# Kernel optimization log

Measured on AMD Instinct MI355X. Metric: run time of the kernel, lower is better.

Reference implementation:

```python
import jax, jax.numpy as jnp
import numpy as np

DIM = 1280
N_HEADS = 10
HEAD_DIM = 128
BASE = 10000.0
BATCH = 2
SEQ = 2048


def _rope(x):
    # x: [b, h, s, d]; matches source: split even/odd channels, rotate, concat halves
    b, h, s, d = x.shape
    theta = 1.0 / (BASE ** (jnp.arange(0, d, 2, dtype=jnp.float32) / d))  # [d/2]
    ang = jnp.arange(s, dtype=jnp.float32)[:, None] * theta               # [s, d/2]
    cos = jnp.cos(ang)
    sin = jnp.sin(ang)
    x1 = x[..., 0::2]
    x2 = x[..., 1::2]
    return jnp.concatenate([x1 * cos - x2 * sin, x1 * sin + x2 * cos], axis=-1)


def setup_inputs() -> dict:
    key = jax.random.key(0)
    ks = jax.random.split(key, 6)
    w_std = 0.02
    x = jax.random.normal(ks[0], (BATCH, SEQ, DIM), dtype=jnp.float32)
    positions = jnp.arange(SEQ, dtype=jnp.int64 if jax.config.jax_enable_x64 else jnp.int32)
    Wq = jax.random.normal(ks[1], (DIM, DIM), dtype=jnp.float32) * w_std
    Wk = jax.random.normal(ks[2], (DIM, DIM), dtype=jnp.float32) * w_std
    Wv = jax.random.normal(ks[3], (DIM, DIM), dtype=jnp.float32) * w_std
    Wo = jax.random.normal(ks[4], (DIM, DIM), dtype=jnp.float32) * w_std
    bq = jnp.zeros((DIM,), jnp.float32)
    bk = jnp.zeros((DIM,), jnp.float32)
    bv = jnp.zeros((DIM,), jnp.float32)
    bo = jnp.zeros((DIM,), jnp.float32)
    return {"x": x, "positions": positions, "Wq": Wq, "bq": bq, "Wk": Wk,
            "bk": bk, "Wv": Wv, "bv": bv, "Wo": Wo, "bo": bo}


def reference(x, positions, Wq, bq, Wk, bk, Wv, bv, Wo, bo):
    b, s, _ = x.shape
    scale = 1.0 / np.sqrt(HEAD_DIM)

    def proj(W, bias):
        y = jnp.einsum('bsd,ed->bse', x, W) + bias  # Linear: x @ W^T + b
        return y.reshape(b, s, N_HEADS, HEAD_DIM).transpose(0, 2, 1, 3)

    q = _rope(proj(Wq, bq))  # [b, h, s, hd]
    k = _rope(proj(Wk, bk))
    v = proj(Wv, bv)

    scores = jnp.einsum('bhqd,bhkd->bhqk', q, k) * scale
    causal = jnp.tril(jnp.ones((s, s), dtype=bool))
    scores = jnp.where(causal, scores, jnp.float32(-jnp.inf))
    attn = jax.nn.softmax(scores, axis=-1)
    out = jnp.einsum('bhqk,bhkd->bhqd', attn, v)
    out = out.transpose(0, 2, 1, 3).reshape(b, s, N_HEADS * HEAD_DIM)
    return jnp.einsum('bse,de->bsd', out, Wo) + bo
```

## Files before the change

### kernel.cpp

```cpp
#include <hip/hip_runtime.h>
#include <cmath>

typedef unsigned short u16;
typedef __attribute__((ext_vector_type(8))) short bf16x8;
typedef __attribute__((ext_vector_type(4))) float f32x4;

#define B_    2
#define SEQ_  2048
#define NH_   10
#define HD_   128
#define DIM_  1280

__device__ __forceinline__ u16 f2bf(float f) {
    union { float f; unsigned u; } v; v.f = f;
    unsigned r = (v.u + 0x7fffu + ((v.u >> 16) & 1u)) >> 16;
    return (u16)r;
}
__device__ __forceinline__ float bf2f(u16 h) {
    union { unsigned u; float f; } v; v.u = ((unsigned)h) << 16;
    return v.f;
}
__device__ __forceinline__ f32x4 mfma16(bf16x8 a, bf16x8 b, f32x4 c) {
    return __builtin_amdgcn_mfma_f32_16x16x32_bf16(a, b, c, 0, 0, 0);
}
__device__ __forceinline__ void g2l16(const void* g, void* l) {
    __builtin_amdgcn_global_load_lds(
        (const __attribute__((address_space(1))) unsigned*)g,
        (__attribute__((address_space(3))) unsigned*)l, 16, 0, 0);
}
__device__ __forceinline__ ushort4 pack4(float a, float b, float c, float d) {
    ushort4 w; w.x = f2bf(a); w.y = f2bf(b); w.z = f2bf(c); w.w = f2bf(d);
    return w;
}

__global__ __launch_bounds__(256) void cvt_k(const float* __restrict__ x,
                                             const float* __restrict__ w0,
                                             const float* __restrict__ w1,
                                             const float* __restrict__ w2,
                                             const float* __restrict__ w3,
                                             u16* __restrict__ xb,
                                             u16* __restrict__ d0,
                                             u16* __restrict__ d1,
                                             u16* __restrict__ d2,
                                             u16* __restrict__ d3,
                                             float* __restrict__ ct,
                                             float* __restrict__ st) {
    const int NX = B_ * SEQ_ * DIM_;
    const int WN = DIM_ * DIM_;
    const int NCV = (NX + 4 * WN) / 8 / 256;
    int bid = blockIdx.x;
    if (bid >= NCV) {
        int idx = (bid - NCV) * 256 + threadIdx.x;
        int s = idx >> 6, j = idx & 63;
        float e = (float)j * (1.0f / 64.0f);
        float theta = 1.0f / powf(10000.0f, e);
        float ang = (float)s * theta;
        ct[idx] = cosf(ang);
        st[idx] = sinf(ang);
        return;
    }
    int i = (bid * 256 + threadIdx.x) * 8;
    const float* src; u16* dst; int off;
    if (i < NX) { src = x; dst = xb; off = i; }
    else {
        int j = i - NX; int w = j / WN; off = j - w * WN;
        src = (w == 0) ? w0 : (w == 1) ? w1 : (w == 2) ? w2 : w3;
        dst = (w == 0) ? d0 : (w == 1) ? d1 : (w == 2) ? d2 : d3;
    }
    float4 a0 = *(const float4*)(src + off);
    float4 a1 = *(const float4*)(src + off + 4);
    union { uint4 q; u16 u[8]; } t;
    t.u[0] = f2bf(a0.x); t.u[1] = f2bf(a0.y);
    t.u[2] = f2bf(a0.z); t.u[3] = f2bf(a0.w);
    t.u[4] = f2bf(a1.x); t.u[5] = f2bf(a1.y);
    t.u[6] = f2bf(a1.z); t.u[7] = f2bf(a1.w);
    *(uint4*)(dst + off) = t.q;
}

template <typename OT>
__device__ __forceinline__ void gemm_core(const u16* __restrict__ A,
                                          const u16* __restrict__ W,
                                          const float* __restrict__ bias,
                                          OT* __restrict__ C,
                                          int m_blk, int n_blk,
                                          u16* As, u16* Bs) {
    const int tid = threadIdx.x;
    const int wave = tid >> 6, lane = tid & 63;
    const int quad = lane >> 4, l16 = lane & 15;
    const int w_m = (wave >> 1) * 64, w_n = (wave & 1) * 64;
    const int srow = wave * 32;
    const int lrow = lane >> 3;
    const int csw = ((lane & 7) ^ lrow) * 8;
    const int rsw = l16 & 7;
    f32x4 acc[4][4] = {};

    const u16* pa = A + (size_t)(m_blk + srow + lrow) * DIM_ + csw;
    const u16* pb = W + (size_t)(n_blk + srow + lrow) * DIM_ + csw;

    for (int k0 = 0; k0 < DIM_; k0 += 64) {
        #pragma unroll
        for (int i = 0; i < 4; ++i) {
            g2l16(pa + k0 + i * 8 * DIM_, As + (srow + i * 8) * 64);
            g2l16(pb + k0 + i * 8 * DIM_, Bs + (srow + i * 8) * 64);
        }
        __syncthreads();
        #pragma unroll
        for (int kk = 0; kk < 2; ++kk) {
            bf16x8 af[4], bf[4];
            #pragma unroll
            for (int mt = 0; mt < 4; ++mt)
                af[mt] = *(const bf16x8*)&As[(w_m + mt * 16 + l16) * 64
                                             + ((kk * 4 + quad) ^ rsw) * 8];
            #pragma unroll
            for (int nt = 0; nt < 4; ++nt)
                bf[nt] = *(const bf16x8*)&Bs[(w_n + nt * 16 + l16) * 64
                                             + ((kk * 4 + quad) ^ rsw) * 8];
            #pragma unroll
            for (int mt = 0; mt < 4; ++mt)
                #pragma unroll
                for (int nt = 0; nt < 4; ++nt)
                    acc[mt][nt] = mfma16(af[mt], bf[nt], acc[mt][nt]);
        }
        __syncthreads();
    }
    #pragma unroll
    for (int nt = 0; nt < 4; ++nt) {
        int col = n_blk + w_n + nt * 16 + l16;
        float bv = bias[col];
        #pragma unroll
        for (int mt = 0; mt < 4; ++mt) {
            #pragma unroll
            for (int r = 0; r < 4; ++r) {
                int row = m_blk + w_m + mt * 16 + quad * 4 + r;
                float v = acc[mt][nt][r] + bv;
                if constexpr (sizeof(OT) == 4) C[(size_t)row * DIM_ + col] = v;
                else C[(size_t)row * DIM_ + col] = (OT)f2bf(v);
            }
        }
    }
}

__global__ __launch_bounds__(256) void qkv_gemm(const u16* __restrict__ xb,
                                                const u16* __restrict__ Wqb,
                                                const u16* __restrict__ Wkb,
                                                const u16* __restrict__ Wvb,
                                                const float* __restrict__ bq,
                                                const float* __restrict__ bk,
                                                const float* __restrict__ bv,
                                                u16* __restrict__ Qb,
                                                u16* __restrict__ Kb,
                                                u16* __restrict__ Vb) {
    __shared__ alignas(16) u16 As[128 * 64];
    __shared__ alignas(16) u16 Bs[128 * 64];
    int id = blockIdx.x;
    int xcd = id & 7, pid = id >> 3;
    int wn = (xcd & 1) * 15 + pid % 15;
    int m  = (xcd >> 1) * 8 + pid / 15;
    int wsel = wn / 10, n_blk = (wn % 10) * 128, m_blk = m * 128;
    const u16* W = (wsel == 0) ? Wqb : (wsel == 1) ? Wkb : Wvb;
    const float* bias = (wsel == 0) ? bq : (wsel == 1) ? bk : bv;
    u16* C = (wsel == 0) ? Qb : (wsel == 1) ? Kb : Vb;
    gemm_core<u16>(xb, W, bias, C, m_blk, n_blk, As, Bs);
}

__global__ __launch_bounds__(256) void out_gemm(const u16* __restrict__ AO,
                                                const u16* __restrict__ Wob,
                                                const float* __restrict__ bo,
                                                float* __restrict__ C) {
    __shared__ alignas(16) u16 As[128 * 64];
    __shared__ alignas(16) u16 Bs[128 * 64];
    int id = blockIdx.x;
    int xcd = id & 7, pid = id >> 3;
    int n = pid % 10;
    int m = xcd * 4 + pid / 10;
    gemm_core<float>(AO, Wob, bo, C, m * 128, n * 128, As, Bs);
}

__global__ __launch_bounds__(256) void rope_k(const u16* __restrict__ Qs_,
                                              const u16* __restrict__ Ks_,
                                              u16* __restrict__ Qd,
                                              u16* __restrict__ Kp,
                                              const float* __restrict__ ct,
                                              const float* __restrict__ st,
                                              float qscale) {
    int t = blockIdx.x * 256 + threadIdx.x;
    const int NR = B_ * SEQ_ * NH_;
    int rid = t >> 3, j0 = (t & 7) * 8;
    const bool isQ = (rid < NR);
    const u16* src = isQ ? Qs_ : Ks_;
    float sc = isQ ? qscale : 1.0f;
    if (!isQ) rid -= NR;
    int h = rid % NH_;
    int s = (rid / NH_) % SEQ_;
    int b = rid / (NH_ * SEQ_);
    const u16* p = src + (size_t)rid * HD_ + 2 * j0;
    union { uint4 q; u16 u[8]; } a0, a1, o1, o2;
    a0.q = *(const uint4*)p;
    a1.q = *(const uint4*)(p + 8);
    const float* cc = ct + (size_t)s * 64 + j0;
    const float* ss = st + (size_t)s * 64 + j0;
    #pragma unroll
    for (int j = 0; j < 8; ++j) {
        float x1 = bf2f((j < 4) ? a0.u[2 * j] : a1.u[2 * j - 8]);
        float x2 = bf2f((j < 4) ? a0.u[2 * j + 1] : a1.u[2 * j - 7]);
        float c = cc[j], sn = ss[j];
        o1.u[j] = f2bf((x1 * c - x2 * sn) * sc);
        o2.u[j] = f2bf((x1 * sn + x2 * c) * sc);
    }
    if (isQ) {
        u16* q = Qd + (size_t)(((size_t)b * SEQ_ + s) * NH_ + h) * HD_;
        *(uint4*)(q + j0) = o1.q;
        *(uint4*)(q + 64 + j0) = o2.q;
    } else {
        int kt = s >> 6, key = s & 63, nt = key >> 4, l16k = key & 15;
        int qd = (j0 >> 3) & 3;
        int kk1 = j0 >> 5, kk2 = 2 + kk1;
        u16* tb = Kp + ((size_t)((b * NH_ + h) * 32 + kt)) * 8192;
        int lane = qd * 16 + l16k;
        *(uint4*)(tb + (kk1 * 4 + nt) * 512 + lane * 8) = o1.q;
        *(uint4*)(tb + (kk2 * 4 + nt) * 512 + lane * 8) = o2.q;
    }
}

__global__ __launch_bounds__(256) void transpose_v(const u16* __restrict__ V,
                                                   u16* __restrict__ Vp) {
    __shared__ u16 T[128][72];
    int stile = blockIdx.x, h = blockIdx.y, b = blockIdx.z;
    int tid = threadIdx.x;
    {
        int sl = tid >> 2, d0 = (tid & 3) * 32;
        const u16* vp = V + ((size_t)((b * SEQ_ + stile * 64 + sl) * NH_ + h)) * HD_ + d0;
        #pragma unroll
        for (int i = 0; i < 4; ++i) {
            union { uint4 q; u16 u[8]; } r;
            r.q = *(const uint4*)(vp + i * 8);
            #pragma unroll
            for (int j = 0; j < 8; ++j) T[d0 + i * 8 + j][sl] = r.u[j];
        }
    }
    __syncthreads();
    {
        int d = tid >> 1, kc = (tid & 1) * 32;
        int dt = d >> 4, l16v = d & 15, kk = kc >> 5;
        u16* tb = Vp + ((size_t)((b * NH_ + h) * 32 + stile)) * 8192 + (kk * 8 + dt) * 512;
        #pragma unroll
        for (int i = 0; i < 4; ++i)
            *(uint4*)(tb + (i * 16 + l16v) * 8) = *(const uint4*)&T[d][kc + i * 8];
    }
}

__device__ const unsigned char QT_TAB[40] =
    {0,1,2,3,4,4,5,5,6,6,7,7,8,8,8,9,9,9,10,10,10,11,11,11,
     12,12,12,12,13,13,13,13,14,14,14,14,15,15,15,15};
__device__ const unsigned char CH_TAB[40] =
    {0,0,0,0,0,1,0,1,0,1,0,1,0,1,2,0,1,2,0,1,2,0,1,2,
     0,1,2,3,0,1,2,3,0,1,2,3,0,1,2,3};

__global__ __launch_bounds__(256, 3) void attn_k(const u16* __restrict__ Q,
                                                 const u16* __restrict__ Kp,
                                                 const u16* __restrict__ Vp,
                                                 u16* __restrict__ AO,
                                                 u16* __restrict__ PO,
                                                 float* __restrict__ Pl) {
    const int cid = blockIdx.x, h = blockIdx.y, b = blockIdx.z;
    const int qt = QT_TAB[cid], c = CH_TAB[cid];
    const int ntiles = 2 * qt + 2;
    const int nch = (ntiles + 7) >> 3;
    const int kt0 = c * 8;
    const int kt1 = (kt0 + 8 < ntiles) ? kt0 + 8 : ntiles;
    const int bh = b * NH_ + h;

    const int tid = threadIdx.x, wave = tid >> 6, lane = tid & 63;
    const int quad = lane >> 4, l16 = lane & 15;

    __shared__ alignas(16) u16 Ks[16 * 512];
    __shared__ alignas(16) u16 Vs[16 * 512];
    __shared__ alignas(16) u16 Pt[4][4][512];

    bf16x8 qf[2][4];
    #pragma unroll
    for (int mt = 0; mt < 2; ++mt) {
        int sq = qt * 128 + wave * 32 + mt * 16 + l16;
        const u16* qp = Q + ((size_t)((b * SEQ_ + sq) * NH_ + h)) * HD_;
        #pragma unroll
        for (int kk = 0; kk < 4; ++kk)
            qf[mt][kk] = *(const bf16x8*)(qp + kk * 32 + quad * 8);
    }
    f32x4 oacc[2][8] = {};
    float l_run[2] = {0.f, 0.f};
    const int q0 = qt * 128 + wave * 32 + l16;

    const u16* kpb = Kp + ((size_t)bh * 32) * 8192;
    const u16* vpb = Vp + ((size_t)bh * 32) * 8192;

    for (int kt = kt0; kt < kt1; ++kt) {
        const u16* kp_t = kpb + (size_t)kt * 8192;
        const u16* vp_t = vpb + (size_t)kt * 8192;
        #pragma unroll
        for (int i = 0; i < 4; ++i) {
            int f = wave * 4 + i;
            g2l16(kp_t + f * 512 + lane * 8, &Ks[f * 512]);
            g2l16(vp_t + f * 512 + lane * 8, &Vs[f * 512]);
        }
        __syncthreads();
        f32x4 sacc[2][4] = {};
        #pragma unroll
        for (int kk = 0; kk < 4; ++kk) {
            #pragma unroll
            for (int nt = 0; nt < 4; ++nt) {
                bf16x8 kf = *(const bf16x8*)&Ks[(kk * 4 + nt) * 512 + lane * 8];
                sacc[0][nt] = mfma16(kf, qf[0][kk], sacc[0][nt]);
                sacc[1][nt] = mfma16(kf, qf[1][kk], sacc[1][nt]);
            }
        }
        const bool maskt = (kt >= 2 * qt);
        const int keyb = kt * 64 + quad * 4;
        #pragma unroll
        for (int mt = 0; mt < 2; ++mt) {
            const int qg = q0 + mt * 16;
            float ps = 0.f;
            #pragma unroll
            for (int nt = 0; nt < 4; ++nt) {
                float p[4];
                #pragma unroll
                for (int r = 0; r < 4; ++r) {
                    float x = sacc[mt][nt][r] - 32.0f;
                    if (maskt && (keyb + nt * 16 + r > qg)) x = -INFINITY;
                    p[r] = __builtin_amdgcn_exp2f(x);
                    ps += p[r];
                }
                ushort4 w4 = pack4(p[0], p[1], p[2], p[3]);
                int rowf = (((nt & 1) << 1) | (quad >> 1)) * 16 + l16;
                *(ushort4*)&Pt[wave][mt * 2 + (nt >> 1)][rowf * 8 + (quad & 1) * 4] = w4;
            }
            l_run[mt] += ps;
        }
        #pragma unroll
        for (int kk = 0; kk < 2; ++kk) {
            bf16x8 pf0 = *(const bf16x8*)&Pt[wave][kk][(quad * 16 + l16) * 8];
            bf16x8 pf1 = *(const bf16x8*)&Pt[wave][2 + kk][(quad * 16 + l16) * 8];
            #pragma unroll
            for (int dt = 0; dt < 8; ++dt) {
                bf16x8 vf = *(const bf16x8*)&Vs[(kk * 8 + dt) * 512 + lane * 8];
                oacc[0][dt] = mfma16(vf, pf0, oacc[0][dt]);
                oacc[1][dt] = mfma16(vf, pf1, oacc[1][dt]);
            }
        }
        __syncthreads();
    }
    #pragma unroll
    for (int mt = 0; mt < 2; ++mt) {
        l_run[mt] += __shfl_xor(l_run[mt], 16, 64);
        l_run[mt] += __shfl_xor(l_run[mt], 32, 64);
    }
    if (nch == 1) {
        #pragma unroll
        for (int mt = 0; mt < 2; ++mt) {
            float invl = 1.0f / l_run[mt];
            int sq = q0 + mt * 16;
            u16* op = AO + ((size_t)((b * SEQ_ + sq) * NH_ + h)) * HD_ + quad * 4;
            #pragma unroll
            for (int dt = 0; dt < 8; ++dt) {
                ushort4 w4 = pack4(oacc[mt][dt][0] * invl, oacc[mt][dt][1] * invl,
                                   oacc[mt][dt][2] * invl, oacc[mt][dt][3] * invl);
                *(ushort4*)(op + dt * 16) = w4;
            }
        }
    } else {
        size_t pidx = ((size_t)bh * 16 + qt) * 4 + c;
        u16* po = PO + pidx * 16384;
        #pragma unroll
        for (int mt = 0; mt < 2; ++mt) {
            #pragma unroll
            for (int dt = 0; dt < 8; ++dt) {
                ushort4 w4 = pack4(oacc[mt][dt][0], oacc[mt][dt][1],
                                   oacc[mt][dt][2], oacc[mt][dt][3]);
                *(ushort4*)(po + ((wave * 16 + mt * 8 + dt) * 64 + lane) * 4) = w4;
            }
            if (quad == 0)
                Pl[pidx * 128 + wave * 32 + mt * 16 + l16] = l_run[mt];
        }
    }
}

__global__ __launch_bounds__(256) void combine_k(const u16* __restrict__ PO,
                                                 const float* __restrict__ Pl,
                                                 u16* __restrict__ AO) {
    const int qt = 4 + blockIdx.x, h = blockIdx.y, b = blockIdx.z;
    const int nch = (2 * qt + 2 + 7) >> 3;
    const int bh = b * NH_ + h;
    const int tid = threadIdx.x;
    const int q = tid >> 1, dh = tid & 1;
    const int wave = q >> 5, mt = (q >> 4) & 1, l16 = q & 15;
    size_t base = ((size_t)bh * 16 + qt) * 4;

    float L = 0.f;
    for (int c = 0; c < nch; ++c) L += Pl[(base + c) * 128 + q];
    float o[64];
    #pragma unroll
    for (int j = 0; j < 64; ++j) o[j] = 0.f;
    for (int c = 0; c < nch; ++c) {
        const u16* p = PO + (base + c) * 16384;
        #pragma unroll
        for (int dtl = 0; dtl < 4; ++dtl) {
            int dt = dh * 4 + dtl;
            #pragma unroll
            for (int quad = 0; quad < 4; ++quad) {
                union { ushort4 v; u16 u[4]; } t;
                t.v = *(const ushort4*)(p + ((wave * 16 + mt * 8 + dt) * 64
                                             + quad * 16 + l16) * 4);
                #pragma unroll
                for (int r = 0; r < 4; ++r)
                    o[dtl * 16 + quad * 4 + r] += bf2f(t.u[r]);
            }
        }
    }
    float invL = 1.0f / L;
    int sq = qt * 128 + q;
    u16* op = AO + ((size_t)((b * SEQ_ + sq) * NH_ + h)) * HD_ + dh * 64;
    union { uint4 v[8]; u16 u[64]; } t;
    #pragma unroll
    for (int j = 0; j < 64; ++j) t.u[j] = f2bf(o[j] * invL);
    #pragma unroll
    for (int i = 0; i < 8; ++i) *(uint4*)(op + i * 8) = t.v[i];
}

extern "C" void kernel_launch(void* const* d_in, const int* in_sizes, int n_in,
                              void* d_out, int out_size, void* d_ws, size_t ws_size,
                              hipStream_t stream) {
    const float* x  = (const float*)d_in[0];
    const float* Wq = (const float*)d_in[2];
    const float* bq = (const float*)d_in[3];
    const float* Wk = (const float*)d_in[4];
    const float* bk = (const float*)d_in[5];
    const float* Wv = (const float*)d_in[6];
    const float* bv = (const float*)d_in[7];
    const float* Wo = (const float*)d_in[8];
    const float* bo = (const float*)d_in[9];
    float* out = (float*)d_out;

    const size_t NE = (size_t)B_ * SEQ_ * NH_ * HD_;
    const size_t WN = (size_t)DIM_ * DIM_;
    u16* Qb  = (u16*)d_ws;
    u16* Kb  = Qb + NE;
    u16* Vb  = Kb + NE;
    u16* Vp  = Vb + NE;
    u16* xb  = Vp + NE;
    u16* Wqb = xb + NE;
    u16* Wkb = Wqb + WN;
    u16* Wvb = Wkb + WN;
    u16* Wob = Wvb + WN;
    float* ct = (float*)(Wob + WN);
    float* st = ct + (size_t)SEQ_ * 64;
    u16* PO  = (u16*)(st + (size_t)SEQ_ * 64);
    float* Pl = (float*)(PO + (size_t)B_ * NH_ * 16 * 4 * 16384);
    u16* Qr = Vb;
    u16* Kp = xb;
    u16* AO = Qb;

    const int NCVT = (B_ * SEQ_ * DIM_ + 4 * (int)WN) / 8 / 256;
    cvt_k<<<NCVT + 512, 256, 0, stream>>>(x, Wq, Wk, Wv, Wo,
                                          xb, Wqb, Wkb, Wvb, Wob, ct, st);

    qkv_gemm<<<dim3(960), 256, 0, stream>>>(xb, Wqb, Wkb, Wvb, bq, bk, bv,
                                            Qb, Kb, Vb);

    transpose_v<<<dim3(SEQ_ / 64, NH_, B_), 256, 0, stream>>>(Vb, Vp);

    const float qsc = 0.08838834764831845f * 1.4426950408889634f;
    rope_k<<<(2 * B_ * SEQ_ * NH_ * 8) / 256, 256, 0, stream>>>(Qb, Kb, Qr, Kp,
                                                                ct, st, qsc);

    attn_k<<<dim3(40, NH_, B_), 256, 0, stream>>>(Qr, Kp, Vp, AO, PO, Pl);
    combine_k<<<dim3(12, NH_, B_), 256, 0, stream>>>(PO, Pl, AO);

    out_gemm<<<dim3(320), 256, 0, stream>>>(AO, Wob, bo, out);
}
```

Measured before the change: 253.3 us.

## Use 256x256 tiles with 8-wave double-buffered pipeline for QKV GEMM

Replaces the 128x128 QKV projection GEMM with a 256x256 tile kernel run by 512 threads (8 waves), with double-buffered LDS (128KB), swizzled layout, async global-to-LDS loads interleaved with MFMA phases, and s_setprio around the compute. The grid drops from 960 to 240 blocks, which raises arithmetic intensity per tile and cuts global/LDS traffic per FLOP. The cost is fewer blocks than CUs on a 256-CU part, so occupancy and load balance may suffer, and the large LDS footprint limits residency.

```diff
diff --git a/kernel.cpp b/kernel.cpp
--- a/kernel.cpp
+++ b/kernel.cpp
@@ -140,27 +140,115 @@
     }
 }
 
-__global__ __launch_bounds__(256) void qkv_gemm(const u16* __restrict__ xb,
-                                                const u16* __restrict__ Wqb,
-                                                const u16* __restrict__ Wkb,
-                                                const u16* __restrict__ Wvb,
-                                                const float* __restrict__ bq,
-                                                const float* __restrict__ bk,
-                                                const float* __restrict__ bv,
-                                                u16* __restrict__ Qb,
-                                                u16* __restrict__ Kb,
-                                                u16* __restrict__ Vb) {
-    __shared__ alignas(16) u16 As[128 * 64];
-    __shared__ alignas(16) u16 Bs[128 * 64];
+__device__ __forceinline__ void gemm256_core(const u16* __restrict__ A,
+                                             const u16* __restrict__ W,
+                                             const float* __restrict__ bias,
+                                             u16* __restrict__ C,
+                                             int m_blk, int n_blk,
+                                             u16* sm) {
+    const int tid = threadIdx.x;
+    const int wave = tid >> 6, lane = tid & 63;
+    const int quad = lane >> 4, l16 = lane & 15;
+    const int wr = wave >> 2, wc = wave & 3;
+    const int rsw = (l16 >> 1) & 3;
+    const int aoff0 = (wr * 128 + l16) * 32 + (quad ^ rsw) * 8;
+    const int boff0 = 16384 + (wc * 64 + l16) * 32 + (quad ^ rsw) * 8;
+    const int csw = ((lane & 3) ^ ((lane >> 3) & 3)) * 8;
+    const int sdst = wave * 1024;
+    const u16* pa = A + (size_t)(m_blk + wave * 32 + (lane >> 2)) * DIM_ + csw;
+    const u16* pb = W + (size_t)(n_blk + wave * 32 + (lane >> 2)) * DIM_ + csw;
+
+    f32x4 acc[8][4] = {};
+
+    #pragma unroll
+    for (int kk = 0; kk < 2; ++kk) {
+        #pragma unroll
+        for (int i = 0; i < 2; ++i) {
+            g2l16(pa + kk * 32 + i * 16 * DIM_, sm + kk * 8192 + sdst + i * 512);
+            g2l16(pb + kk * 32 + i * 16 * DIM_,
+                  sm + 16384 + kk * 8192 + sdst + i * 512);
+        }
+    }
+    asm volatile("s_waitcnt vmcnt(4)" ::: "memory");
+    __builtin_amdgcn_s_barrier();
+
+    const int NT = DIM_ / 64;
+    bf16x8 bf[4];
+    for (int t = 0; t < NT; ++t) {
+        const int cur = (t & 1) * 32768, nxt = cur ^ 32768;
+        const bool st = (t + 1 < NT);
+        const u16* pat = pa + (t + 1) * 64;
+        const u16* pbt = pb + (t + 1) * 64;
+        #pragma unroll
+        for (int ph = 0; ph < 4; ++ph) {
+            const int kk = ph >> 1, mh = ph & 1;
+            if (mh == 0) {
+                #pragma unroll
+                for (int nt = 0; nt < 4; ++nt)
+                    bf[nt] = *(const bf16x8*)&sm[cur + boff0 + kk * 8192 + nt * 512];
+            }
+            bf16x8 af[4];
+            #pragma unroll
+            for (int i = 0; i < 4; ++i)
+                af[i] = *(const bf16x8*)&sm[cur + aoff0 + kk * 8192
+                                            + (mh * 4 + i) * 512];
+            if (st) {
+                const u16* ps = (mh == 0) ? pat : pbt;
+                #pragma unroll
+                for (int i = 0; i < 2; ++i)
+                    g2l16(ps + kk * 32 + i * 16 * DIM_,
+                          sm + nxt + mh * 16384 + kk * 8192 + sdst + i * 512);
+            }
+            __builtin_amdgcn_s_barrier();
+            asm volatile("s_waitcnt lgkmcnt(0)" ::: "memory");
+            __builtin_amdgcn_s_setprio(1);
+            #pragma unroll
+            for (int i = 0; i < 4; ++i)
+                #pragma unroll
+                for (int nt = 0; nt < 4; ++nt)
+                    acc[mh * 4 + i][nt] = mfma16(af[i], bf[nt], acc[mh * 4 + i][nt]);
+            __builtin_amdgcn_s_setprio(0);
+            if (ph & 1) {
+                if (st) asm volatile("s_waitcnt vmcnt(4)" ::: "memory");
+                else if (ph == 1) asm volatile("s_waitcnt vmcnt(0)" ::: "memory");
+            }
+            __builtin_amdgcn_s_barrier();
+        }
+    }
+    #pragma unroll
+    for (int nt = 0; nt < 4; ++nt) {
+        int col = n_blk + wc * 64 + nt * 16 + l16;
+        float bv = bias[col];
+        #pragma unroll
+        for (int mt = 0; mt < 8; ++mt) {
+            int row = m_blk + wr * 128 + mt * 16 + quad * 4;
+            #pragma unroll
+            for (int r = 0; r < 4; ++r)
+                C[(size_t)(row + r) * DIM_ + col] = f2bf(acc[mt][nt][r] + bv);
+        }
+    }
+}
+
+__global__ __launch_bounds__(512, 2) void qkv_gemm(const u16* __restrict__ xb,
+                                                   const u16* __restrict__ Wqb,
+                                                   const u16* __restrict__ Wkb,
+                                                   const u16* __restrict__ Wvb,
+                                                   const float* __restrict__ bq,
+                                                   const float* __restrict__ bk,
+                                                   const float* __restrict__ bv,
+                                                   u16* __restrict__ Qb,
+                                                   u16* __restrict__ Kb,
+                                                   u16* __restrict__ Vb) {
+    __shared__ alignas(16) u16 sm[65536];
     int id = blockIdx.x;
     int xcd = id & 7, pid = id >> 3;
-    int wn = (xcd & 1) * 15 + pid % 15;
-    int m  = (xcd >> 1) * 8 + pid / 15;
-    int wsel = wn / 10, n_blk = (wn % 10) * 128, m_blk = m * 128;
+    int m = xcd * 2 + pid / 15;
+    int ns = pid % 15;
+    int wsel = ns / 5, n_blk = (ns % 5) * 256;
     const u16* W = (wsel == 0) ? Wqb : (wsel == 1) ? Wkb : Wvb;
     const float* bias = (wsel == 0) ? bq : (wsel == 1) ? bk : bv;
     u16* C = (wsel == 0) ? Qb : (wsel == 1) ? Kb : Vb;
-    gemm_core<u16>(xb, W, bias, C, m_blk, n_blk, As, Bs);
+    gemm256_core(xb, W, bias, C, m * 256, n_blk, sm);
 }
 
 __global__ __launch_bounds__(256) void out_gemm(const u16* __restrict__ AO,
@@ -462,7 +550,7 @@
     cvt_k<<<NCVT + 512, 256, 0, stream>>>(x, Wq, Wk, Wv, Wo,
                                           xb, Wqb, Wkb, Wvb, Wob, ct, st);
 
-    qkv_gemm<<<dim3(960), 256, 0, stream>>>(xb, Wqb, Wkb, Wvb, bq, bk, bv,
+    qkv_gemm<<<dim3(240), 512, 0, stream>>>(xb, Wqb, Wkb, Wvb, bq, bk, bv,
                                             Qb, Kb, Vb);
 
     transpose_v<<<dim3(SEQ_ / 64, NH_, B_), 256, 0, stream>>>(Vb, Vp);
```

New measurement: 250.0 us. About the same (-1.3%).
